# Optimization experiments

Hardware: AMD Instinct MI355X
Metric: run time of the kernel (lower is better)

## Reference

```python
import jax, jax.numpy as jnp
import numpy as np

N = 50000   # nodes
F = 128     # num_features (per branch)
E = 800000  # edges
G = 16      # graphs in batch
T = 3       # blocks per branch


def setup_inputs() -> dict:
    key = jax.random.key(0)
    ks = jax.random.split(key, 32)
    s = 0.05
    d = {}
    d["x"] = jax.random.normal(ks[0], (N, 2 * F), jnp.float32)
    d["edge_index"] = jax.random.randint(ks[1], (2, E), 0, N)
    d["edge_weight"] = jax.random.uniform(ks[2], (E,), jnp.float32)
    d["batch"] = jnp.sort(jax.random.randint(ks[3], (N,), 0, G))
    d["states"] = jax.random.randint(ks[4], (N,), 0, 2).astype(jnp.float32)

    def w(k, shape):
        return jax.random.normal(k, shape, jnp.float32) * s

    for i, p in enumerate(["p1", "p2"]):
        b = 5 + i * 5
        d[f"{p}_a0"] = w(ks[b], (T,))            # alpha0: Linear(1,1,bias=False) weight per block
        d[f"{p}_a1W"] = w(ks[b + 1], (T, F, F))    # alpha1 weight
        d[f"{p}_a1b"] = w(ks[b + 2], (T, F))       # alpha1 bias
        d[f"{p}_linW"] = w(ks[b + 3], (T, F, F))   # conv.lin weight
        d[f"{p}_linb"] = w(ks[b + 4], (T, F))      # conv.lin bias
    d["beta0_W"] = w(ks[15], (F, F))
    d["beta1_W"] = w(ks[16], (F, F))
    d["beta2_W"] = w(ks[17], (F, 2 * F))
    d["beta2_b"] = w(ks[18], (F,))
    d["gamma0_W"] = w(ks[19], (F, F))
    d["gamma1_W"] = w(ks[20], (F, F))
    d["gamma2_W"] = w(ks[21], (F, F))
    d["gamma3_W"] = w(ks[22], (3 * F // 2, 3 * F))
    d["gamma4_W"] = w(ks[23], (1, 3 * F // 2))
    d["gamma4_b"] = w(ks[24], (1,))
    return d


def _lrelu(v):
    return jax.nn.leaky_relu(v, 0.2)


def _block(x, states, a0, a1W, a1b, linW, linb, src, dst, ew):
    # x = lrelu(alpha1(x + alpha0(states)))
    h = _lrelu((x + states[:, None] * a0) @ a1W.T + a1b)
    # CustomGCNConv: lin then edge-weighted gather/scatter-add (source->target)
    h = h @ linW.T + linb
    msg = ew[:, None] * h[src]  # [E, F]
    return jax.ops.segment_sum(msg, dst, num_segments=x.shape[0])


def reference(x, edge_index, edge_weight, batch, states,
              p1_a0, p1_a1W, p1_a1b, p1_linW, p1_linb,
              p2_a0, p2_a1W, p2_a1b, p2_linW, p2_linb,
              beta0_W, beta1_W, beta2_W, beta2_b,
              gamma0_W, gamma1_W, gamma2_W, gamma3_W, gamma4_W, gamma4_b):
    Fh = x.shape[1] // 2
    x1, x2 = x[:, :Fh], x[:, Fh:]
    s0, s1 = edge_index[0], edge_index[1]
    x1s = jnp.zeros_like(x1)
    x2s = jnp.zeros_like(x2)
    for t in range(T):
        # branch1 uses reversed edges edge_index[[1,0]]
        x1 = _lrelu(_block(x1, states, p1_a0[t], p1_a1W[t], p1_a1b[t],
                           p1_linW[t], p1_linb[t], s1, s0, edge_weight))
        x2 = _lrelu(_block(x2, states, p2_a0[t], p2_a1W[t], p2_a1b[t],
                           p2_linW[t], p2_linb[t], s0, s1, edge_weight))
        x1s = x1s + x1
        x2s = x2s + x2
    xc = _lrelu(jnp.concatenate([x1s @ beta0_W.T, x2s @ beta1_W.T], -1) @ beta2_W.T + beta2_b)
    sel = (states == 1.0)[:, None]
    # per-graph pooled sums broadcast back to nodes (== repeat_interleave since batch is sorted)
    x_s = jax.ops.segment_sum(jnp.where(sel, xc, 0.0), batch, num_segments=G)[batch]
    x_sum = jax.ops.segment_sum(xc, batch, num_segments=G)[batch]
    h = jnp.concatenate([xc @ gamma0_W.T, x_s @ gamma1_W.T, x_sum @ gamma2_W.T], -1)
    h = _lrelu(h @ gamma3_W.T)
    return (h @ gamma4_W.T + gamma4_b).reshape(-1)
```

## Files before the change

kernel.cpp:

```cpp
#include <hip/hip_runtime.h>

typedef short s8v __attribute__((ext_vector_type(8)));
typedef float f32x4 __attribute__((ext_vector_type(4)));

#define LRELU(v) ((v) > 0.f ? (v) : 0.2f * (v))

constexpr int NBK = 391;
constexpr int TILE = 8192;
constexpr int CAP = 4096;

__device__ __forceinline__ float b2f(unsigned short b) {
  return __uint_as_float(((unsigned int)b) << 16);
}
__device__ __forceinline__ unsigned short f2b(float f) {
  unsigned int x = __float_as_uint(f);
  x += 0x7fffu + ((x >> 16) & 1u);
  return (unsigned short)(x >> 16);
}
__device__ __forceinline__ unsigned int pack2(float lo, float hi) {
  return ((unsigned int)f2b(hi) << 16) | (unsigned int)f2b(lo);
}

struct FArgs {
  const unsigned short* X[2];
  const unsigned short* W1[2];
  const float* b1[2];
  const float* a0p[2];
  const float* rowsum[2];
  const unsigned short* W2[2];
  const float* b2[2];
  unsigned short* H[2];
  const float* states;
  int N;
};

__global__ __launch_bounds__(256) void fused_mlp_kernel(FArgs fa)
{
  __shared__ __align__(16) unsigned short Ws[128 * 128];
  __shared__ __align__(16) unsigned short Tp[128 * 128];
  const int d = blockIdx.y;
  const int tid = threadIdx.x;
  const int lane = tid & 63;
  const int w = tid >> 6;
  const int l15 = lane & 15;
  const int g = lane >> 4;
  const int m0 = blockIdx.x * 128;
  const int N = fa.N;

#pragma unroll
  for (int j = 0; j < 8; ++j) {
    int idx = tid + j * 256;
    int o = idx >> 4, c = idx & 15;
    uint4 v = *(const uint4*)(fa.W1[d] + (size_t)o * 128 + c * 8);
    *(uint4*)&Ws[o * 128 + (c ^ (o & 15)) * 8] = v;
  }
  s8v a[2][4];
#pragma unroll
  for (int mf = 0; mf < 2; ++mf) {
    int row = m0 + w * 32 + mf * 16 + l15;
    const unsigned short* ar = fa.X[d] + (size_t)row * 128 + g * 8;
#pragma unroll
    for (int ks = 0; ks < 4; ++ks) {
      s8v t = {};
      if (row < N) t = *(const s8v*)(ar + ks * 32);
      a[mf][ks] = t;
    }
  }
  f32x4 zero4 = {0.f, 0.f, 0.f, 0.f};
  f32x4 acc[2][8];
#pragma unroll
  for (int mf = 0; mf < 2; ++mf)
#pragma unroll
    for (int nf = 0; nf < 8; ++nf) acc[mf][nf] = zero4;
  __syncthreads();
#pragma unroll
  for (int ks = 0; ks < 4; ++ks) {
#pragma unroll
    for (int nf = 0; nf < 8; ++nf) {
      int c = ks * 4 + g;
      s8v b = *(const s8v*)&Ws[(nf * 16 + l15) * 128 + (c ^ l15) * 8];
      acc[0][nf] = __builtin_amdgcn_mfma_f32_16x16x32_bf16(a[0][ks], b, acc[0][nf], 0, 0, 0);
      acc[1][nf] = __builtin_amdgcn_mfma_f32_16x16x32_bf16(a[1][ks], b, acc[1][nf], 0, 0, 0);
    }
  }
  const float a0 = fa.a0p[d][0];
#pragma unroll
  for (int mf = 0; mf < 2; ++mf) {
#pragma unroll
    for (int r = 0; r < 4; ++r) {
      int lrow = w * 32 + mf * 16 + g * 4 + r;
      int row = m0 + lrow;
      float sa = (row < N) ? fa.states[row] * a0 : 0.f;
#pragma unroll
      for (int nf = 0; nf < 8; ++nf) {
        int col = nf * 16 + l15;
        float v = 0.f;
        if (row < N) {
          v = acc[mf][nf][r] + fa.b1[d][col] + sa * fa.rowsum[d][col];
          v = LRELU(v);
        }
        int cch = col >> 3;
        Tp[lrow * 128 + ((cch ^ (lrow & 15)) << 3) + (col & 7)] = f2b(v);
      }
    }
  }
  __syncthreads();
#pragma unroll
  for (int j = 0; j < 8; ++j) {
    int idx = tid + j * 256;
    int o = idx >> 4, c = idx & 15;
    uint4 v = *(const uint4*)(fa.W2[d] + (size_t)o * 128 + c * 8);
    *(uint4*)&Ws[o * 128 + (c ^ (o & 15)) * 8] = v;
  }
  __syncthreads();
#pragma unroll
  for (int mf = 0; mf < 2; ++mf) {
    int lrow = w * 32 + mf * 16 + l15;
#pragma unroll
    for (int ks = 0; ks < 4; ++ks) {
      int c2 = ks * 4 + g;
      a[mf][ks] = *(const s8v*)&Tp[lrow * 128 + ((c2 ^ (lrow & 15)) << 3)];
    }
  }
#pragma unroll
  for (int mf = 0; mf < 2; ++mf)
#pragma unroll
    for (int nf = 0; nf < 8; ++nf) acc[mf][nf] = zero4;
#pragma unroll
  for (int ks = 0; ks < 4; ++ks) {
#pragma unroll
    for (int nf = 0; nf < 8; ++nf) {
      int c = ks * 4 + g;
      s8v b = *(const s8v*)&Ws[(nf * 16 + l15) * 128 + (c ^ l15) * 8];
      acc[0][nf] = __builtin_amdgcn_mfma_f32_16x16x32_bf16(a[0][ks], b, acc[0][nf], 0, 0, 0);
      acc[1][nf] = __builtin_amdgcn_mfma_f32_16x16x32_bf16(a[1][ks], b, acc[1][nf], 0, 0, 0);
    }
  }
#pragma unroll
  for (int mf = 0; mf < 2; ++mf) {
#pragma unroll
    for (int r = 0; r < 4; ++r) {
      int row = m0 + w * 32 + mf * 16 + g * 4 + r;
      if (row >= N) continue;
      unsigned short* crow = fa.H[d] + (size_t)row * 128;
#pragma unroll
      for (int nf = 0; nf < 8; ++nf) {
        int col = nf * 16 + l15;
        crow[col] = f2b(acc[mf][nf][r] + fa.b2[d][col]);
      }
    }
  }
}

struct PBArgs {
  const unsigned short* U1; const unsigned short* U2;
  const unsigned short* Wb0; const unsigned short* Wb1;
  const unsigned short* Wb2;
  const float* bias;
  unsigned short* XC;
  int N;
};

__global__ __launch_bounds__(256) void fused_beta_kernel(PBArgs pa)
{
  __shared__ __align__(16) unsigned short Ws[128 * 128];
  __shared__ __align__(16) unsigned short Tp[128 * 256];
  const int tid = threadIdx.x;
  const int lane = tid & 63;
  const int w = tid >> 6;
  const int l15 = lane & 15;
  const int g = lane >> 4;
  const int m0 = blockIdx.x * 128;
  const int N = pa.N;
  f32x4 zero4 = {0.f, 0.f, 0.f, 0.f};
  s8v a[2][4];
  f32x4 acc[2][8];

#pragma unroll
  for (int ph = 0; ph < 2; ++ph) {
    const unsigned short* Wsrc = ph ? pa.Wb1 : pa.Wb0;
    const unsigned short* Usrc = ph ? pa.U2 : pa.U1;
#pragma unroll
    for (int j = 0; j < 8; ++j) {
      int idx = tid + j * 256;
      int o = idx >> 4, c = idx & 15;
      uint4 v = *(const uint4*)(Wsrc + (size_t)o * 128 + c * 8);
      *(uint4*)&Ws[o * 128 + (c ^ (o & 15)) * 8] = v;
    }
#pragma unroll
    for (int mf = 0; mf < 2; ++mf) {
      int row = m0 + w * 32 + mf * 16 + l15;
      const unsigned short* ar = Usrc + (size_t)row * 128 + g * 8;
#pragma unroll
      for (int ks = 0; ks < 4; ++ks) {
        s8v t = {};
        if (row < N) t = *(const s8v*)(ar + ks * 32);
        a[mf][ks] = t;
      }
    }
#pragma unroll
    for (int mf = 0; mf < 2; ++mf)
#pragma unroll
      for (int nf = 0; nf < 8; ++nf) acc[mf][nf] = zero4;
    __syncthreads();
#pragma unroll
    for (int ks = 0; ks < 4; ++ks) {
#pragma unroll
      for (int nf = 0; nf < 8; ++nf) {
        int c = ks * 4 + g;
        s8v b = *(const s8v*)&Ws[(nf * 16 + l15) * 128 + (c ^ l15) * 8];
        acc[0][nf] = __builtin_amdgcn_mfma_f32_16x16x32_bf16(a[0][ks], b, acc[0][nf], 0, 0, 0);
        acc[1][nf] = __builtin_amdgcn_mfma_f32_16x16x32_bf16(a[1][ks], b, acc[1][nf], 0, 0, 0);
      }
    }
#pragma unroll
    for (int mf = 0; mf < 2; ++mf) {
#pragma unroll
      for (int r = 0; r < 4; ++r) {
        int lrow = w * 32 + mf * 16 + g * 4 + r;
        int row = m0 + lrow;
#pragma unroll
        for (int nf = 0; nf < 8; ++nf) {
          int col = nf * 16 + l15;
          float v = (row < N) ? acc[mf][nf][r] : 0.f;
          int cch = (ph << 4) + (col >> 3);
          Tp[lrow * 256 + ((cch ^ (lrow & 15)) << 3) + (col & 7)] = f2b(v);
        }
      }
    }
    __syncthreads();
  }

  f32x4 accf[2][8];
#pragma unroll
  for (int mf = 0; mf < 2; ++mf)
#pragma unroll
    for (int nf = 0; nf < 8; ++nf) accf[mf][nf] = zero4;
#pragma unroll
  for (int half = 0; half < 2; ++half) {
#pragma unroll
    for (int j = 0; j < 8; ++j) {
      int idx = tid + j * 256;
      int o = idx >> 4, c = idx & 15;
      uint4 v = *(const uint4*)(pa.Wb2 + (size_t)o * 256 + half * 128 + c * 8);
      *(uint4*)&Ws[o * 128 + (c ^ (o & 15)) * 8] = v;
    }
#pragma unroll
    for (int mf = 0; mf < 2; ++mf) {
      int lrow = w * 32 + mf * 16 + l15;
#pragma unroll
      for (int ks = 0; ks < 4; ++ks) {
        int cch = (half << 4) + ks * 4 + g;
        a[mf][ks] = *(const s8v*)&Tp[lrow * 256 + ((cch ^ (lrow & 15)) << 3)];
      }
    }
    __syncthreads();
#pragma unroll
    for (int ks = 0; ks < 4; ++ks) {
#pragma unroll
      for (int nf = 0; nf < 8; ++nf) {
        int c = ks * 4 + g;
        s8v b = *(const s8v*)&Ws[(nf * 16 + l15) * 128 + (c ^ l15) * 8];
        accf[0][nf] = __builtin_amdgcn_mfma_f32_16x16x32_bf16(a[0][ks], b, accf[0][nf], 0, 0, 0);
        accf[1][nf] = __builtin_amdgcn_mfma_f32_16x16x32_bf16(a[1][ks], b, accf[1][nf], 0, 0, 0);
      }
    }
    __syncthreads();
  }
#pragma unroll
  for (int mf = 0; mf < 2; ++mf) {
#pragma unroll
    for (int r = 0; r < 4; ++r) {
      int row = m0 + w * 32 + mf * 16 + g * 4 + r;
      if (row >= N) continue;
      unsigned short* crow = pa.XC + (size_t)row * 128;
#pragma unroll
      for (int nf = 0; nf < 8; ++nf) {
        int col = nf * 16 + l15;
        float v = accf[mf][nf][r] + pa.bias[col];
        crow[col] = f2b(LRELU(v));
      }
    }
  }
}

__global__ __launch_bounds__(256) void g3_kernel(
    const unsigned short* __restrict__ xc,
    const unsigned short* __restrict__ A16,
    const unsigned short* __restrict__ B16,
    const int* __restrict__ batch,
    const unsigned short* __restrict__ W0,
    const unsigned short* __restrict__ W3,
    const float* __restrict__ g4W,
    const float* __restrict__ g4b,
    float* __restrict__ out, int N)
{
  constexpr int NF = 12;
  __shared__ __align__(16) unsigned short Ws[192 * 128];
  __shared__ __align__(16) unsigned short Tp[128 * 128];
  const int tid = threadIdx.x;
  const int lane = tid & 63;
  const int w = tid >> 6;
  const int l15 = lane & 15;
  const int g = lane >> 4;
  const int m0 = blockIdx.x * 128;

  f32x4 zero4 = {0.f, 0.f, 0.f, 0.f};
  s8v a[2][4];

#pragma unroll
  for (int j = 0; j < 8; ++j) {
    int idx = tid + j * 256;
    int o = idx >> 4, c = idx & 15;
    uint4 v = *(const uint4*)(W0 + (size_t)o * 128 + c * 8);
    *(uint4*)&Ws[o * 128 + (c ^ (o & 15)) * 8] = v;
  }
#pragma unroll
  for (int mf = 0; mf < 2; ++mf) {
    int row = m0 + w * 32 + mf * 16 + l15;
    const unsigned short* ar = xc + (size_t)row * 128 + g * 8;
#pragma unroll
    for (int ks = 0; ks < 4; ++ks) {
      s8v t = {};
      if (row < N) t = *(const s8v*)(ar + ks * 32);
      a[mf][ks] = t;
    }
  }
  {
    f32x4 acc1[2][8];
#pragma unroll
    for (int mf = 0; mf < 2; ++mf)
#pragma unroll
      for (int nf = 0; nf < 8; ++nf) acc1[mf][nf] = zero4;
    __syncthreads();
#pragma unroll
    for (int ks = 0; ks < 4; ++ks) {
#pragma unroll
      for (int nf = 0; nf < 8; ++nf) {
        int c = ks * 4 + g;
        s8v b = *(const s8v*)&Ws[(nf * 16 + l15) * 128 + (c ^ l15) * 8];
        acc1[0][nf] = __builtin_amdgcn_mfma_f32_16x16x32_bf16(a[0][ks], b, acc1[0][nf], 0, 0, 0);
        acc1[1][nf] = __builtin_amdgcn_mfma_f32_16x16x32_bf16(a[1][ks], b, acc1[1][nf], 0, 0, 0);
      }
    }
#pragma unroll
    for (int mf = 0; mf < 2; ++mf) {
#pragma unroll
      for (int r = 0; r < 4; ++r) {
        int lrow = w * 32 + mf * 16 + g * 4 + r;
        int row = m0 + lrow;
#pragma unroll
        for (int nf = 0; nf < 8; ++nf) {
          int col = nf * 16 + l15;
          float v = (row < N) ? acc1[mf][nf][r] : 0.f;
          int cch = col >> 3;
          Tp[lrow * 128 + ((cch ^ (lrow & 15)) << 3) + (col & 7)] = f2b(v);
        }
      }
    }
  }
  __syncthreads();

  f32x4 acc[2][NF];
#pragma unroll
  for (int mf = 0; mf < 2; ++mf)
#pragma unroll
    for (int nf = 0; nf < NF; ++nf) acc[mf][nf] = zero4;

  int brow[2];
#pragma unroll
  for (int mf = 0; mf < 2; ++mf) {
    int row = m0 + w * 32 + mf * 16 + l15;
    brow[mf] = (row < N) ? batch[row] : 0;
  }

  for (int kk = 0; kk < 384; kk += 128) {
#pragma unroll
    for (int j = 0; j < NF; ++j) {
      int idx = tid + j * 256;
      int o = idx >> 4, c = idx & 15;
      uint4 v = *(const uint4*)(W3 + (size_t)o * 384 + kk + c * 8);
      *(uint4*)&Ws[o * 128 + (c ^ (o & 15)) * 8] = v;
    }
    if (kk == 0) {
#pragma unroll
      for (int mf = 0; mf < 2; ++mf) {
        int lrow = w * 32 + mf * 16 + l15;
#pragma unroll
        for (int ks = 0; ks < 4; ++ks) {
          int c2 = ks * 4 + g;
          a[mf][ks] = *(const s8v*)&Tp[lrow * 128 + ((c2 ^ (lrow & 15)) << 3)];
        }
      }
    } else {
#pragma unroll
      for (int mf = 0; mf < 2; ++mf) {
        int row = m0 + w * 32 + mf * 16 + l15;
        const unsigned short* ar = ((kk == 128) ? A16 : B16) + (size_t)brow[mf] * 128 + g * 8;
#pragma unroll
        for (int ks = 0; ks < 4; ++ks) {
          s8v t = {};
          if (row < N) t = *(const s8v*)(ar + ks * 32);
          a[mf][ks] = t;
        }
      }
    }
    __syncthreads();
#pragma unroll
    for (int ks = 0; ks < 4; ++ks) {
#pragma unroll
      for (int nf = 0; nf < NF; ++nf) {
        int c = ks * 4 + g;
        s8v b = *(const s8v*)&Ws[(nf * 16 + l15) * 128 + (c ^ l15) * 8];
        acc[0][nf] = __builtin_amdgcn_mfma_f32_16x16x32_bf16(a[0][ks], b, acc[0][nf], 0, 0, 0);
        acc[1][nf] = __builtin_amdgcn_mfma_f32_16x16x32_bf16(a[1][ks], b, acc[1][nf], 0, 0, 0);
      }
    }
    if (kk < 256) __syncthreads();
  }

  float w4[NF];
#pragma unroll
  for (int nf = 0; nf < NF; ++nf) w4[nf] = g4W[nf * 16 + l15];
  const float gb = g4b[0];

#pragma unroll
  for (int mf = 0; mf < 2; ++mf) {
#pragma unroll
    for (int r = 0; r < 4; ++r) {
      int row = m0 + w * 32 + mf * 16 + g * 4 + r;
      float dot = 0.f;
#pragma unroll
      for (int nf = 0; nf < NF; ++nf) {
        float v = acc[mf][nf][r];
        v = LRELU(v);
        dot += v * w4[nf];
      }
#pragma unroll
      for (int m = 1; m < 16; m <<= 1) dot += __shfl_xor(dot, m, 16);
      if (l15 == 0 && row < N) out[row] = dot + gb;
    }
  }
}

struct CJobs { const float* s[9]; unsigned short* d[9]; int n[9]; };
__global__ void convert_kernel(CJobs jb) {
  int j = blockIdx.y;
  int idx = (blockIdx.x * 256 + threadIdx.x) * 8;
  if (idx >= jb.n[j]) return;
  const float* s = jb.s[j] + idx;
  float4 p0 = *(const float4*)s;
  float4 p1 = *(const float4*)(s + 4);
  uint4 u;
  u.x = pack2(p0.x, p0.y); u.y = pack2(p0.z, p0.w);
  u.z = pack2(p1.x, p1.y); u.w = pack2(p1.z, p1.w);
  *(uint4*)(jb.d[j] + idx) = u;
}

__global__ void rowsum_kernel(const float* __restrict__ a1,
                              const float* __restrict__ a2, float* __restrict__ rs) {
  int j = blockIdx.x;
  const float* src = (j < 3) ? (a1 + (size_t)j * 16384) : (a2 + (size_t)(j - 3) * 16384);
  int o = threadIdx.x;
  float s = 0.f;
  for (int k = 0; k < 128; ++k) s += src[o * 128 + k];
  rs[j * 128 + o] = s;
}

__global__ void init_kernel(const float* __restrict__ x,
                            unsigned short* __restrict__ x1, unsigned short* __restrict__ x2,
                            int n)
{
  int idx = blockIdx.x * blockDim.x + threadIdx.x;
  int total = n * 16;
  for (; idx < total; idx += gridDim.x * blockDim.x) {
    int r = idx >> 4, c = idx & 15;
    const float* xr = x + (size_t)r * 256 + c * 8;
    float4 p0 = *(const float4*)xr;
    float4 p1 = *(const float4*)(xr + 4);
    uint4 u1;
    u1.x = pack2(p0.x, p0.y); u1.y = pack2(p0.z, p0.w);
    u1.z = pack2(p1.x, p1.y); u1.w = pack2(p1.z, p1.w);
    float4 q0 = *(const float4*)(xr + 128);
    float4 q1 = *(const float4*)(xr + 132);
    uint4 u2;
    u2.x = pack2(q0.x, q0.y); u2.y = pack2(q0.z, q0.w);
    u2.z = pack2(q1.x, q1.y); u2.w = pack2(q1.z, q1.w);
    ((uint4*)(x1 + (size_t)r * 128))[c] = u1;
    ((uint4*)(x2 + (size_t)r * 128))[c] = u2;
  }
}

struct BinArgs {
  const int* s0; const int* s1; const float* ew;
  int* bcur0; int* bcur1;
  unsigned long long* bin0; unsigned long long* bin1;
  int E;
};
__global__ __launch_bounds__(256) void bin_kernel(BinArgs ba)
{
  __shared__ int hist0[NBK], hist1[NBK];
  __shared__ int base0[NBK], base1[NBK];
  const int t = threadIdx.x;
  const int e0 = blockIdx.x * TILE;
  const int e1 = min(e0 + TILE, ba.E);
  for (int i = t; i < NBK; i += 256) { hist0[i] = 0; hist1[i] = 0; }
  __syncthreads();
  for (int e = e0 + t; e < e1; e += 256) {
    atomicAdd(&hist0[ba.s0[e] >> 7], 1);
    atomicAdd(&hist1[ba.s1[e] >> 7], 1);
  }
  __syncthreads();
  for (int i = t; i < NBK; i += 256) {
    int c0 = hist0[i];
    base0[i] = c0 ? atomicAdd(&ba.bcur0[i], c0) : 0;
    int c1 = hist1[i];
    base1[i] = c1 ? atomicAdd(&ba.bcur1[i], c1) : 0;
  }
  __syncthreads();
  for (int i = t; i < NBK; i += 256) { hist0[i] = 0; hist1[i] = 0; }
  __syncthreads();
  for (int e = e0 + t; e < e1; e += 256) {
    int d0 = ba.s0[e], d1 = ba.s1[e];
    unsigned long long wb = (unsigned long long)__float_as_uint(ba.ew[e]) << 32;
    int b0 = d0 >> 7, b1 = d1 >> 7;
    int r0 = base0[b0] + atomicAdd(&hist0[b0], 1);
    if (r0 < CAP)
      ba.bin0[(size_t)b0 * CAP + r0] = wb | (unsigned int)((d0 & 127) << 16) | (unsigned int)d1;
    int r1 = base1[b1] + atomicAdd(&hist1[b1], 1);
    if (r1 < CAP)
      ba.bin1[(size_t)b1 * CAP + r1] = wb | (unsigned int)((d1 & 127) << 16) | (unsigned int)d0;
  }
}

struct BScanArgs { const int* cnt[2]; int* bbase[2]; };
__global__ __launch_bounds__(128) void bscan_kernel(BScanArgs a)
{
  __shared__ int ld[2][NBK];
  int wid = threadIdx.x >> 6, lane = threadIdx.x & 63;
  for (int i = lane; i < NBK; i += 64) ld[wid][i] = a.cnt[wid][i];
  __syncthreads();
  if (lane == 0) {
    int acc = 0;
    for (int i = 0; i < NBK; ++i) { int v = ld[wid][i]; ld[wid][i] = acc; acc += v; }
    a.bbase[wid][NBK] = acc;
  }
  __syncthreads();
  for (int i = lane; i < NBK; i += 64) a.bbase[wid][i] = ld[wid][i];
}

struct RArgs {
  const int* bbase[2];
  const unsigned long long* bin[2];
  unsigned int* comb[2];
  int* row[2];
  int n;
};
__global__ __launch_bounds__(256) void reorder_kernel(RArgs ra)
{
  const int d = blockIdx.y;
  const int b = blockIdx.x;
  const unsigned long long* __restrict__ bin = ra.bin[d] + (size_t)b * CAP;
  unsigned int* __restrict__ comb = ra.comb[d];
  int* __restrict__ row = ra.row[d];
  const int nb = b * 128;
  const int ne = min(nb + 128, ra.n);
  const int t = threadIdx.x;
  __shared__ int lcnt[128];
  __shared__ int lcur[128];
  __shared__ int wtot[4];
  if (t < 128) lcnt[t] = 0;
  const int span_beg = ra.bbase[d][b];
  const int span_end = ra.bbase[d][b + 1];
  const int cnt = span_end - span_beg;
  __syncthreads();
  for (int i = t; i < cnt; i += 256) {
    int nl = ((unsigned int)bin[i] >> 16) & 127;
    atomicAdd(&lcnt[nl], 1);
  }
  __syncthreads();
  int lane = t & 63, wv = t >> 6;
  int v = (t < 128) ? lcnt[t] : 0;
  int sc = v;
#pragma unroll
  for (int off = 1; off < 64; off <<= 1) {
    int u = __shfl_up(sc, off, 64);
    if (lane >= off) sc += u;
  }
  if (lane == 63) wtot[wv] = sc;
  __syncthreads();
  int excl = sc - v + ((wv == 1) ? wtot[0] : 0);
  if (t < 128) {
    lcur[t] = excl;
    if (nb + t < ne) row[nb + t] = span_beg + excl;
  }
  if (b == NBK - 1 && t == 0) row[ra.n] = span_end;
  __syncthreads();
  for (int i = t; i < cnt; i += 256) {
    unsigned long long r = bin[i];
    unsigned int lo = (unsigned int)r;
    float w = __uint_as_float((unsigned int)(r >> 32));
    int nl = (lo >> 16) & 127;
    int slot = atomicAdd(&lcur[nl], 1);
    comb[span_beg + slot] = (lo & 0xffffu) | ((unsigned int)f2b(w) << 16);
  }
}

struct GArgs {
  const int* rowstart[2];
  const unsigned int* comb[2];
  const unsigned short* h[2];
  unsigned short* xout[2];
  const unsigned int* add1[2];
  const unsigned int* add2[2];
  int n;
};
__global__ void gather_kernel(GArgs ga)
{
  int gw = blockIdx.x * (blockDim.x >> 6) + (threadIdx.x >> 6);
  int lane = threadIdx.x & 63;
  if (gw >= 2 * ga.n) return;
  int dir = (gw >= ga.n) ? 1 : 0;
  int node = gw - dir * ga.n;
  const int* __restrict__ rowstart = ga.rowstart[dir];
  const unsigned int* __restrict__ comb = ga.comb[dir];
  const unsigned int* __restrict__ h = (const unsigned int*)ga.h[dir];
  int beg = rowstart[node], end = rowstart[node + 1];
  float a0 = 0.f, a1 = 0.f;
  for (int p = beg; p < end; p += 16) {
    unsigned int cc[16];
    unsigned int uu[16];
#pragma unroll
    for (int i = 0; i < 16; ++i) {
      int pi = p + i;
      cc[i] = (pi < end) ? comb[pi] : 0u;
    }
#pragma unroll
    for (int i = 0; i < 16; ++i)
      uu[i] = h[(size_t)(cc[i] & 0xffffu) * 64 + lane];
#pragma unroll
    for (int i = 0; i < 16; ++i) {
      float wv = b2f((unsigned short)(cc[i] >> 16));
      a0 += wv * b2f((unsigned short)uu[i]);
      a1 += wv * b2f((unsigned short)(uu[i] >> 16));
    }
  }
  float v0 = LRELU(a0), v1 = LRELU(a1);
  unsigned int* xo = (unsigned int*)(ga.xout[dir] + (size_t)node * 128);
  if (ga.add1[0]) {
    unsigned int ua = ga.add1[dir][(size_t)node * 64 + lane];
    unsigned int ub = ga.add2[dir][(size_t)node * 64 + lane];
    v0 += b2f((unsigned short)ua) + b2f((unsigned short)ub);
    v1 += b2f((unsigned short)(ua >> 16)) + b2f((unsigned short)(ub >> 16));
  }
  xo[lane] = pack2(v0, v1);
}

__global__ __launch_bounds__(256) void segsum_kernel(
    const unsigned short* __restrict__ xc, const int* __restrict__ batch,
    const float* __restrict__ states,
    float* __restrict__ gsel, float* __restrict__ gsum, int n)
{
  int slot = threadIdx.x >> 6;
  int lane = threadIdx.x & 63;
  int r0 = blockIdx.x * 128 + slot * 32;
  if (r0 >= n) return;
  int r1 = min(r0 + 32, n);
  const unsigned int* __restrict__ xcu = (const unsigned int*)xc;
  float sel0 = 0.f, sel1 = 0.f, sum0 = 0.f, sum1 = 0.f;
  int cur = batch[r0];
  for (int r = r0; r < r1; r += 4) {
    unsigned int u[4]; int bb[4]; float st[4];
#pragma unroll
    for (int i = 0; i < 4; ++i) {
      int ri = min(r + i, r1 - 1);
      u[i] = xcu[(size_t)ri * 64 + lane];
      bb[i] = batch[ri];
      st[i] = states[ri];
    }
    int m = min(4, r1 - r);
#pragma unroll
    for (int i = 0; i < 4; ++i) {
      if (i >= m) break;
      if (bb[i] != cur) {
        atomicAdd(&gsel[cur * 128 + lane * 2], sel0);
        atomicAdd(&gsel[cur * 128 + lane * 2 + 1], sel1);
        atomicAdd(&gsum[cur * 128 + lane * 2], sum0);
        atomicAdd(&gsum[cur * 128 + lane * 2 + 1], sum1);
        sel0 = sel1 = sum0 = sum1 = 0.f;
        cur = bb[i];
      }
      float lo = b2f((unsigned short)u[i]);
      float hi = b2f((unsigned short)(u[i] >> 16));
      sum0 += lo; sum1 += hi;
      if (st[i] == 1.0f) { sel0 += lo; sel1 += hi; }
    }
  }
  atomicAdd(&gsel[cur * 128 + lane * 2], sel0);
  atomicAdd(&gsel[cur * 128 + lane * 2 + 1], sel1);
  atomicAdd(&gsum[cur * 128 + lane * 2], sum0);
  atomicAdd(&gsum[cur * 128 + lane * 2 + 1], sum1);
}

__global__ void small16_kernel(const float* __restrict__ gsel, const float* __restrict__ gsum,
                               const float* __restrict__ g1W, const float* __restrict__ g2W,
                               unsigned short* __restrict__ A16, unsigned short* __restrict__ B16)
{
  int r = blockIdx.x, t = threadIdx.x, o = t & 127;
  const float* src = (t < 128) ? gsel : gsum;
  const float* Wm  = (t < 128) ? g1W : g2W;
  float acc = 0.f;
  for (int k = 0; k < 128; ++k) acc += src[r * 128 + k] * Wm[o * 128 + k];
  unsigned short* dst = (t < 128) ? A16 : B16;
  dst[r * 128 + o] = f2b(acc);
}

extern "C" void kernel_launch(void* const* d_in, const int* in_sizes, int n_in,
                              void* d_out, int out_size, void* d_ws, size_t ws_size,
                              hipStream_t stream)
{
  const int N = 50000, F = 128, E = 800000, G = 16, T = 3;
  const float* x      = (const float*)d_in[0];
  const int*   ei     = (const int*)d_in[1];
  const int*   s0     = ei;
  const int*   s1     = ei + E;
  const float* ew     = (const float*)d_in[2];
  const int*   batch  = (const int*)d_in[3];
  const float* states = (const float*)d_in[4];
  const float* p_a0[2]   = {(const float*)d_in[5],  (const float*)d_in[10]};
  const float* p_a1W[2]  = {(const float*)d_in[6],  (const float*)d_in[11]};
  const float* p_a1b[2]  = {(const float*)d_in[7],  (const float*)d_in[12]};
  const float* p_linW[2] = {(const float*)d_in[8],  (const float*)d_in[13]};
  const float* p_linb[2] = {(const float*)d_in[9],  (const float*)d_in[14]};
  const float* beta0W = (const float*)d_in[15];
  const float* beta1W = (const float*)d_in[16];
  const float* beta2W = (const float*)d_in[17];
  const float* beta2b = (const float*)d_in[18];
  const float* g0W = (const float*)d_in[19];
  const float* g1W = (const float*)d_in[20];
  const float* g2W = (const float*)d_in[21];
  const float* g3W = (const float*)d_in[22];
  const float* g4W = (const float*)d_in[23];
  const float* g4b = (const float*)d_in[24];
  float* out = (float*)d_out;

  char* p = (char*)d_ws;
  auto alloc = [&](size_t bytes) {
    char* r = p;
    p += (bytes + 255) & ~(size_t)255;
    return r;
  };
  const size_t NFb2 = (size_t)N * F * sizeof(unsigned short);
  unsigned short* X1[3] = {(unsigned short*)alloc(NFb2), (unsigned short*)alloc(NFb2),
                           (unsigned short*)alloc(NFb2)};
  unsigned short* X2[3] = {(unsigned short*)alloc(NFb2), (unsigned short*)alloc(NFb2),
                           (unsigned short*)alloc(NFb2)};
  unsigned short* TMP0 = (unsigned short*)alloc(NFb2);
  unsigned short* TMP1 = (unsigned short*)alloc(NFb2);
  unsigned short* HH0  = (unsigned short*)alloc(NFb2);
  unsigned short* HH1  = (unsigned short*)alloc(NFb2);
  int*   row0 = (int*)alloc((size_t)(N + 1) * 4);
  int*   row1 = (int*)alloc((size_t)(N + 1) * 4);
  int*   bbase0 = (int*)alloc((size_t)(NBK + 1) * 4);
  int*   bbase1 = (int*)alloc((size_t)(NBK + 1) * 4);
  int*   bcur0 = (int*)alloc((size_t)NBK * 4);
  int*   bcur1 = (int*)alloc((size_t)NBK * 4);
  unsigned long long* bin0 = (unsigned long long*)alloc((size_t)NBK * CAP * 8);
  unsigned long long* bin1 = (unsigned long long*)alloc((size_t)NBK * CAP * 8);
  unsigned int* comb0 = (unsigned int*)alloc((size_t)E * 4);
  unsigned int* comb1 = (unsigned int*)alloc((size_t)E * 4);
  float* gsel = (float*)alloc((size_t)G * F * 4);
  float* gsum = (float*)alloc((size_t)G * F * 4);
  unsigned short* A16b = (unsigned short*)alloc((size_t)G * F * 2);
  unsigned short* B16b = (unsigned short*)alloc((size_t)G * F * 2);
  unsigned short* wreg = (unsigned short*)alloc((size_t)352256 * 2);
  float* rs = (float*)alloc((size_t)6 * 128 * 4);

  unsigned short* a1Wb[2]  = {wreg + 0,      wreg + 49152};
  unsigned short* linWb[2] = {wreg + 98304,  wreg + 147456};
  unsigned short* b0b = wreg + 196608;
  unsigned short* b1b = wreg + 212992;
  unsigned short* b2b = wreg + 229376;
  unsigned short* g0b = wreg + 262144;
  unsigned short* g3b = wreg + 278528;

  const dim3 blk256(256);
  const int GX = (N + 127) / 128;
  const int EB = (E + TILE - 1) / TILE;

  hipMemsetAsync(bcur0, 0, (size_t)NBK * 4, stream);
  hipMemsetAsync(bcur1, 0, (size_t)NBK * 4, stream);
  BinArgs bna;
  bna.s0 = s0; bna.s1 = s1; bna.ew = ew;
  bna.bcur0 = bcur0; bna.bcur1 = bcur1;
  bna.bin0 = bin0; bna.bin1 = bin1;
  bna.E = E;
  bin_kernel<<<EB, blk256, 0, stream>>>(bna);
  BScanArgs bsa;
  bsa.cnt[0] = bcur0; bsa.cnt[1] = bcur1;
  bsa.bbase[0] = bbase0; bsa.bbase[1] = bbase1;
  bscan_kernel<<<1, 128, 0, stream>>>(bsa);
  RArgs ra;
  ra.bbase[0] = bbase0; ra.bbase[1] = bbase1;
  ra.bin[0] = bin0; ra.bin[1] = bin1;
  ra.comb[0] = comb0; ra.comb[1] = comb1;
  ra.row[0] = row0; ra.row[1] = row1;
  ra.n = N;
  reorder_kernel<<<dim3(NBK, 2), blk256, 0, stream>>>(ra);

  CJobs jb;
  jb.s[0] = p_a1W[0];  jb.d[0] = a1Wb[0];  jb.n[0] = 49152;
  jb.s[1] = p_a1W[1];  jb.d[1] = a1Wb[1];  jb.n[1] = 49152;
  jb.s[2] = p_linW[0]; jb.d[2] = linWb[0]; jb.n[2] = 49152;
  jb.s[3] = p_linW[1]; jb.d[3] = linWb[1]; jb.n[3] = 49152;
  jb.s[4] = beta0W;    jb.d[4] = b0b;      jb.n[4] = 16384;
  jb.s[5] = beta1W;    jb.d[5] = b1b;      jb.n[5] = 16384;
  jb.s[6] = beta2W;    jb.d[6] = b2b;      jb.n[6] = 32768;
  jb.s[7] = g0W;       jb.d[7] = g0b;      jb.n[7] = 16384;
  jb.s[8] = g3W;       jb.d[8] = g3b;      jb.n[8] = 73728;
  convert_kernel<<<dim3(36, 9), blk256, 0, stream>>>(jb);
  rowsum_kernel<<<6, 128, 0, stream>>>(p_a1W[0], p_a1W[1], rs);
  init_kernel<<<3125, blk256, 0, stream>>>(x, X1[0], X2[0], N);

  for (int t = 0; t < T; ++t) {
    int rv = t % 3, wv = (t + 1) % 3;

    FArgs fa;
    fa.X[0] = X1[rv];  fa.X[1] = X2[rv];
    fa.W1[0] = a1Wb[0] + t * 16384;  fa.W1[1] = a1Wb[1] + t * 16384;
    fa.b1[0] = p_a1b[0] + t * F;     fa.b1[1] = p_a1b[1] + t * F;
    fa.a0p[0] = p_a0[0] + t;         fa.a0p[1] = p_a0[1] + t;
    fa.rowsum[0] = rs + t * 128;     fa.rowsum[1] = rs + (3 + t) * 128;
    fa.W2[0] = linWb[0] + t * 16384; fa.W2[1] = linWb[1] + t * 16384;
    fa.b2[0] = p_linb[0] + t * F;    fa.b2[1] = p_linb[1] + t * F;
    fa.H[0] = HH0;  fa.H[1] = HH1;
    fa.states = states;  fa.N = N;
    fused_mlp_kernel<<<dim3(GX, 2), blk256, 0, stream>>>(fa);

    GArgs ga;
    ga.rowstart[0] = row0; ga.rowstart[1] = row1;
    ga.comb[0] = comb0;    ga.comb[1] = comb1;
    ga.h[0] = HH0;         ga.h[1] = HH1;
    if (t == T - 1) {
      ga.xout[0] = TMP0;  ga.xout[1] = TMP1;
      ga.add1[0] = (const unsigned int*)X1[1];  ga.add1[1] = (const unsigned int*)X2[1];
      ga.add2[0] = (const unsigned int*)X1[2];  ga.add2[1] = (const unsigned int*)X2[2];
    } else {
      ga.xout[0] = X1[wv];  ga.xout[1] = X2[wv];
      ga.add1[0] = nullptr; ga.add1[1] = nullptr;
      ga.add2[0] = nullptr; ga.add2[1] = nullptr;
    }
    ga.n = N;
    gather_kernel<<<(2 * N + 3) / 4, blk256, 0, stream>>>(ga);
  }

  PBArgs pb;
  pb.U1 = TMP0; pb.U2 = TMP1;
  pb.Wb0 = b0b; pb.Wb1 = b1b; pb.Wb2 = b2b;
  pb.bias = beta2b; pb.XC = HH0; pb.N = N;
  fused_beta_kernel<<<GX, blk256, 0, stream>>>(pb);

  hipMemsetAsync(gsel, 0, (size_t)G * F * 4, stream);
  hipMemsetAsync(gsum, 0, (size_t)G * F * 4, stream);
  segsum_kernel<<<GX, blk256, 0, stream>>>(HH0, batch, states, gsel, gsum, N);
  small16_kernel<<<G, blk256, 0, stream>>>(gsel, gsum, g1W, g2W, A16b, B16b);

  g3_kernel<<<GX, blk256, 0, stream>>>(HH0, A16b, B16b, batch, g0b, g3b, g4W, g4b, out, N);
}
```

Baseline: 456.0 us.

## Gather two nodes per wavefront with 8-byte loads, shrink beta LDS, fold memsets

The gather kernel now has each half-wavefront (32 lanes) handle one destination node, loading 4 bf16 features per lane with uint2 loads. Edge chunks are 8 instead of 16, and the loop count is taken as the max over the paired node. This is meant to cut wasted lanes and raise the bytes per load for the row gathers, at the cost of divergence between paired nodes of unequal degree. The fused beta kernel interleaves each branch GEMM with its half of the beta2 GEMM, halving the Tp shared buffer, which may improve occupancy. The two gsel/gsum memsets are folded into bscan_kernel to remove launches.

Measured after the change: 442.7 us. 2.9% less time.

```diff
diff --git a/kernel.cpp b/kernel.cpp
--- a/kernel.cpp
+++ b/kernel.cpp
@@ -153,8 +153,8 @@
 }
 
 struct PBArgs {
-  const unsigned short* U1; const unsigned short* U2;
-  const unsigned short* Wb0; const unsigned short* Wb1;
+  const unsigned short* U[2];
+  const unsigned short* Wb[2];
   const unsigned short* Wb2;
   const float* bias;
   unsigned short* XC;
@@ -164,7 +164,7 @@
 __global__ __launch_bounds__(256) void fused_beta_kernel(PBArgs pa)
 {
   __shared__ __align__(16) unsigned short Ws[128 * 128];
-  __shared__ __align__(16) unsigned short Tp[128 * 256];
+  __shared__ __align__(16) unsigned short Tp[128 * 128];
   const int tid = threadIdx.x;
   const int lane = tid & 63;
   const int w = tid >> 6;
@@ -174,23 +174,24 @@
   const int N = pa.N;
   f32x4 zero4 = {0.f, 0.f, 0.f, 0.f};
   s8v a[2][4];
-  f32x4 acc[2][8];
-
-#pragma unroll
+  f32x4 accf[2][8];
+#pragma unroll
+  for (int mf = 0; mf < 2; ++mf)
+#pragma unroll
+    for (int nf = 0; nf < 8; ++nf) accf[mf][nf] = zero4;
+
   for (int ph = 0; ph < 2; ++ph) {
-    const unsigned short* Wsrc = ph ? pa.Wb1 : pa.Wb0;
-    const unsigned short* Usrc = ph ? pa.U2 : pa.U1;
 #pragma unroll
     for (int j = 0; j < 8; ++j) {
       int idx = tid + j * 256;
       int o = idx >> 4, c = idx & 15;
-      uint4 v = *(const uint4*)(Wsrc + (size_t)o * 128 + c * 8);
+      uint4 v = *(const uint4*)(pa.Wb[ph] + (size_t)o * 128 + c * 8);
       *(uint4*)&Ws[o * 128 + (c ^ (o & 15)) * 8] = v;
     }
 #pragma unroll
     for (int mf = 0; mf < 2; ++mf) {
       int row = m0 + w * 32 + mf * 16 + l15;
-      const unsigned short* ar = Usrc + (size_t)row * 128 + g * 8;
+      const unsigned short* ar = pa.U[ph] + (size_t)row * 128 + g * 8;
 #pragma unroll
       for (int ks = 0; ks < 4; ++ks) {
         s8v t = {};
@@ -198,6 +199,7 @@
         a[mf][ks] = t;
       }
     }
+    f32x4 acc[2][8];
 #pragma unroll
     for (int mf = 0; mf < 2; ++mf)
 #pragma unroll
@@ -213,6 +215,7 @@
         acc[1][nf] = __builtin_amdgcn_mfma_f32_16x16x32_bf16(a[1][ks], b, acc[1][nf], 0, 0, 0);
       }
     }
+    __syncthreads();
 #pragma unroll
     for (int mf = 0; mf < 2; ++mf) {
 #pragma unroll
@@ -223,26 +226,17 @@
         for (int nf = 0; nf < 8; ++nf) {
           int col = nf * 16 + l15;
           float v = (row < N) ? acc[mf][nf][r] : 0.f;
-          int cch = (ph << 4) + (col >> 3);
-          Tp[lrow * 256 + ((cch ^ (lrow & 15)) << 3) + (col & 7)] = f2b(v);
+          int cch = col >> 3;
+          Tp[lrow * 128 + ((cch ^ (lrow & 15)) << 3) + (col & 7)] = f2b(v);
         }
       }
     }
     __syncthreads();
-  }
-
-  f32x4 accf[2][8];
-#pragma unroll
-  for (int mf = 0; mf < 2; ++mf)
-#pragma unroll
-    for (int nf = 0; nf < 8; ++nf) accf[mf][nf] = zero4;
-#pragma unroll
-  for (int half = 0; half < 2; ++half) {
 #pragma unroll
     for (int j = 0; j < 8; ++j) {
       int idx = tid + j * 256;
       int o = idx >> 4, c = idx & 15;
-      uint4 v = *(const uint4*)(pa.Wb2 + (size_t)o * 256 + half * 128 + c * 8);
+      uint4 v = *(const uint4*)(pa.Wb2 + (size_t)o * 256 + ph * 128 + c * 8);
       *(uint4*)&Ws[o * 128 + (c ^ (o & 15)) * 8] = v;
     }
 #pragma unroll
@@ -250,8 +244,8 @@
       int lrow = w * 32 + mf * 16 + l15;
 #pragma unroll
       for (int ks = 0; ks < 4; ++ks) {
-        int cch = (half << 4) + ks * 4 + g;
-        a[mf][ks] = *(const s8v*)&Tp[lrow * 256 + ((cch ^ (lrow & 15)) << 3)];
+        int c2 = ks * 4 + g;
+        a[mf][ks] = *(const s8v*)&Tp[lrow * 128 + ((c2 ^ (lrow & 15)) << 3)];
       }
     }
     __syncthreads();
@@ -533,11 +527,12 @@
   }
 }
 
-struct BScanArgs { const int* cnt[2]; int* bbase[2]; };
+struct BScanArgs { const int* cnt[2]; int* bbase[2]; float* gsel; float* gsum; };
 __global__ __launch_bounds__(128) void bscan_kernel(BScanArgs a)
 {
   __shared__ int ld[2][NBK];
   int wid = threadIdx.x >> 6, lane = threadIdx.x & 63;
+  for (int i = threadIdx.x; i < 2048; i += 128) { a.gsel[i] = 0.f; a.gsum[i] = 0.f; }
   for (int i = lane; i < NBK; i += 64) ld[wid][i] = a.cnt[wid][i];
   __syncthreads();
   if (lane == 0) {
@@ -617,43 +612,59 @@
 };
 __global__ void gather_kernel(GArgs ga)
 {
-  int gw = blockIdx.x * (blockDim.x >> 6) + (threadIdx.x >> 6);
+  int pair = blockIdx.x * (blockDim.x >> 6) + (threadIdx.x >> 6);
   int lane = threadIdx.x & 63;
-  if (gw >= 2 * ga.n) return;
-  int dir = (gw >= ga.n) ? 1 : 0;
-  int node = gw - dir * ga.n;
+  int sub = lane >> 5;
+  int fl = lane & 31;
+  long long gnode = (long long)2 * pair + sub;
+  bool valid = gnode < 2 * ga.n;
+  int dir = (valid && gnode >= ga.n) ? 1 : 0;
+  int node = valid ? (int)(gnode - (long long)dir * ga.n) : 0;
   const int* __restrict__ rowstart = ga.rowstart[dir];
   const unsigned int* __restrict__ comb = ga.comb[dir];
   const unsigned int* __restrict__ h = (const unsigned int*)ga.h[dir];
   int beg = rowstart[node], end = rowstart[node + 1];
-  float a0 = 0.f, a1 = 0.f;
-  for (int p = beg; p < end; p += 16) {
-    unsigned int cc[16];
-    unsigned int uu[16];
-#pragma unroll
-    for (int i = 0; i < 16; ++i) {
-      int pi = p + i;
+  if (!valid) end = beg;
+  int nch_own = (end - beg + 7) >> 3;
+  int nch_oth = __shfl_xor(nch_own, 32, 64);
+  int nch = max(nch_own, nch_oth);
+  float a0 = 0.f, a1 = 0.f, a2 = 0.f, a3 = 0.f;
+  for (int ch = 0; ch < nch; ++ch) {
+    int p0 = beg + ch * 8;
+    unsigned int cc[8];
+    uint2 uu[8];
+#pragma unroll
+    for (int i = 0; i < 8; ++i) {
+      int pi = p0 + i;
       cc[i] = (pi < end) ? comb[pi] : 0u;
     }
 #pragma unroll
-    for (int i = 0; i < 16; ++i)
-      uu[i] = h[(size_t)(cc[i] & 0xffffu) * 64 + lane];
-#pragma unroll
-    for (int i = 0; i < 16; ++i) {
+    for (int i = 0; i < 8; ++i)
+      uu[i] = *(const uint2*)(h + (size_t)(cc[i] & 0xffffu) * 64 + fl * 2);
+#pragma unroll
+    for (int i = 0; i < 8; ++i) {
       float wv = b2f((unsigned short)(cc[i] >> 16));
-      a0 += wv * b2f((unsigned short)uu[i]);
-      a1 += wv * b2f((unsigned short)(uu[i] >> 16));
-    }
-  }
-  float v0 = LRELU(a0), v1 = LRELU(a1);
-  unsigned int* xo = (unsigned int*)(ga.xout[dir] + (size_t)node * 128);
+      a0 += wv * b2f((unsigned short)uu[i].x);
+      a1 += wv * b2f((unsigned short)(uu[i].x >> 16));
+      a2 += wv * b2f((unsigned short)uu[i].y);
+      a3 += wv * b2f((unsigned short)(uu[i].y >> 16));
+    }
+  }
+  float v0 = LRELU(a0), v1 = LRELU(a1), v2 = LRELU(a2), v3 = LRELU(a3);
   if (ga.add1[0]) {
-    unsigned int ua = ga.add1[dir][(size_t)node * 64 + lane];
-    unsigned int ub = ga.add2[dir][(size_t)node * 64 + lane];
-    v0 += b2f((unsigned short)ua) + b2f((unsigned short)ub);
-    v1 += b2f((unsigned short)(ua >> 16)) + b2f((unsigned short)(ub >> 16));
-  }
-  xo[lane] = pack2(v0, v1);
+    uint2 ua = ((const uint2*)ga.add1[dir])[(size_t)node * 32 + fl];
+    uint2 ub = ((const uint2*)ga.add2[dir])[(size_t)node * 32 + fl];
+    v0 += b2f((unsigned short)ua.x) + b2f((unsigned short)ub.x);
+    v1 += b2f((unsigned short)(ua.x >> 16)) + b2f((unsigned short)(ub.x >> 16));
+    v2 += b2f((unsigned short)ua.y) + b2f((unsigned short)ub.y);
+    v3 += b2f((unsigned short)(ua.y >> 16)) + b2f((unsigned short)(ub.y >> 16));
+  }
+  if (valid) {
+    uint2 o;
+    o.x = pack2(v0, v1);
+    o.y = pack2(v2, v3);
+    ((uint2*)(ga.xout[dir] + (size_t)node * 128))[fl] = o;
+  }
 }
 
 __global__ __launch_bounds__(256) void segsum_kernel(
@@ -799,6 +810,7 @@
   BScanArgs bsa;
   bsa.cnt[0] = bcur0; bsa.cnt[1] = bcur1;
   bsa.bbase[0] = bbase0; bsa.bbase[1] = bbase1;
+  bsa.gsel = gsel; bsa.gsum = gsum;
   bscan_kernel<<<1, 128, 0, stream>>>(bsa);
   RArgs ra;
   ra.bbase[0] = bbase0; ra.bbase[1] = bbase1;
@@ -851,17 +863,15 @@
       ga.add2[0] = nullptr; ga.add2[1] = nullptr;
     }
     ga.n = N;
-    gather_kernel<<<(2 * N + 3) / 4, blk256, 0, stream>>>(ga);
+    gather_kernel<<<(2 * N + 7) / 8, blk256, 0, stream>>>(ga);
   }
 
   PBArgs pb;
-  pb.U1 = TMP0; pb.U2 = TMP1;
-  pb.Wb0 = b0b; pb.Wb1 = b1b; pb.Wb2 = b2b;
+  pb.U[0] = TMP0; pb.U[1] = TMP1;
+  pb.Wb[0] = b0b; pb.Wb[1] = b1b; pb.Wb2 = b2b;
   pb.bias = beta2b; pb.XC = HH0; pb.N = N;
   fused_beta_kernel<<<GX, blk256, 0, stream>>>(pb);
 
-  hipMemsetAsync(gsel, 0, (size_t)G * F * 4, stream);
-  hipMemsetAsync(gsum, 0, (size_t)G * F * 4, stream);
   segsum_kernel<<<GX, blk256, 0, stream>>>(HH0, batch, states, gsel, gsum, N);
   small16_kernel<<<G, blk256, 0, stream>>>(gsel, gsum, g1W, g2W, A16b, B16b);
 
```
